# Optimization experiments

Hardware: AMD Instinct MI355X
Metric: run time of the kernel (lower is better)

Reference implementation:

```python
import jax, jax.numpy as jnp
import numpy as np
from jax import lax

D, C, H, W = 4, 64, 64, 64
QK = 32  # q/k projection channels


def _conv3x3(x, w, b):
    # x: [D,C,H,W], w: [O,I,3,3] -> [D,O,H,W], SAME padding, stride 1
    y = lax.conv_general_dilated(x, w, window_strides=(1, 1), padding='SAME',
                                 dimension_numbers=('NCHW', 'OIHW', 'NCHW'))
    return y + b[None, :, None, None]


def setup_inputs() -> dict:
    key = jax.random.key(0)
    ks = jax.random.split(key, 6)
    x = jax.random.normal(ks[0], (D, C, H, W), dtype=jnp.float32)
    atten = jax.random.normal(ks[1], (D, H * W, H * W), dtype=jnp.float32)
    q_w = jax.random.normal(ks[2], (QK, C, 3, 3), dtype=jnp.float32) * 0.05
    q_b = jax.random.normal(ks[3], (QK,), dtype=jnp.float32) * 0.05
    k_w = jax.random.normal(ks[4], (QK, C, 3, 3), dtype=jnp.float32) * 0.05
    k_b = jax.random.normal(ks[5], (QK,), dtype=jnp.float32) * 0.05
    gamma = jnp.ones((1,), dtype=jnp.float32)
    return {"x": x, "atten": atten, "q_w": q_w, "q_b": q_b,
            "k_w": k_w, "k_b": k_b, "gamma": gamma}


def reference(x, atten, q_w, q_b, k_w, k_b, gamma):
    d, c, h, w = x.shape
    n = h * w
    q = _conv3x3(x, q_w, q_b).reshape(d, QK, n)   # [D,32,N]
    k = _conv3x3(x, k_w, k_b).reshape(d, QK, n)   # [D,32,N]
    v = x.reshape(d, c, n)                         # [D,C,N]
    # attention = softmax(q^T k), then softmax(attention + atten) -- double softmax
    attn = jax.nn.softmax(jnp.einsum('dcn,dcm->dnm', q, k), axis=-1)  # [D,N,N]
    attn = jax.nn.softmax(attn + atten, axis=-1)
    # out = v @ attn^T  -> [D,C,N]
    out = jnp.einsum('dcm,dnm->dcn', v, attn).reshape(d, c, h, w)
    return gamma * out + x
```

## Files before the change

### kernel.cpp

```cpp
#include <hip/hip_runtime.h>
#include <hip/hip_bf16.h>

typedef float  f32x4  __attribute__((ext_vector_type(4)));
typedef short  s16x4  __attribute__((ext_vector_type(4)));
typedef short  s16x8  __attribute__((ext_vector_type(8)));
typedef __bf16 bf16x8 __attribute__((ext_vector_type(8)));

#define N_PIX 4096

__device__ __forceinline__ unsigned short f2bf(float f) {
    __hip_bfloat16 h = __float2bfloat16(f);
    return *reinterpret_cast<unsigned short*>(&h);
}
__device__ __forceinline__ float bf2f(unsigned short u) {
    __hip_bfloat16 h;
    *reinterpret_cast<unsigned short*>(&h) = u;
    return __bfloat162float(h);
}

#if __has_builtin(__builtin_amdgcn_mfma_f32_16x16x16bf16_1k)
#define USE_K16 1
#else
#define USE_K16 0
#endif

__device__ __forceinline__ f32x4 mac_k32(s16x4 alo, s16x4 ahi, s16x4 blo, s16x4 bhi, f32x4 c) {
#if USE_K16
    c = __builtin_amdgcn_mfma_f32_16x16x16bf16_1k(alo, blo, c, 0, 0, 0);
    c = __builtin_amdgcn_mfma_f32_16x16x16bf16_1k(ahi, bhi, c, 0, 0, 0);
#else
    s16x8 a8 = __builtin_shufflevector(alo, ahi, 0, 1, 2, 3, 4, 5, 6, 7);
    s16x8 b8 = __builtin_shufflevector(blo, bhi, 0, 1, 2, 3, 4, 5, 6, 7);
    c = __builtin_amdgcn_mfma_f32_16x16x32_bf16(__builtin_bit_cast(bf16x8, a8),
                                                __builtin_bit_cast(bf16x8, b8), c, 0, 0, 0);
#endif
    return c;
}

__global__ __launch_bounds__(256) void to_bf16_kernel(const float* __restrict__ x,
                                                      unsigned short* __restrict__ v_bf) {
    int i = blockIdx.x * 256 + threadIdx.x;
    v_bf[i] = f2bf(x[i]);
}

__global__ __launch_bounds__(256) void pad_kernel(const float* __restrict__ x,
                                                  float* __restrict__ xp) {
    int i = blockIdx.x * 256 + threadIdx.x;
    int xx = i % 66;
    int t  = i / 66;
    int yy = t % 66;
    int cd = t / 66;
    float v = 0.f;
    if (xx >= 1 && xx <= 64 && yy >= 1 && yy <= 64)
        v = x[(size_t)cd * 4096 + (yy - 1) * 64 + (xx - 1)];
    xp[i] = v;
}

__global__ __launch_bounds__(256) void conv_qk_kernel(
    const float* __restrict__ xp,
    const float* __restrict__ q_w, const float* __restrict__ q_b,
    const float* __restrict__ k_w, const float* __restrict__ k_b,
    unsigned short* __restrict__ qTp_hi, unsigned short* __restrict__ qTp_lo,
    unsigned short* __restrict__ kTp_hi, unsigned short* __restrict__ kTp_lo) {
    int bid = blockIdx.x;
    int d  = bid >> 9;
    int o  = __builtin_amdgcn_readfirstlane((bid >> 4) & 31);
    int yg = bid & 15;
    int tid = threadIdx.x;
    int y   = yg * 4 + (tid >> 6);
    int col = tid & 63;
    const float* xc0 = xp + (size_t)d * (64 * 4356) + y * 66 + col;
    const float* wq = q_w + o * 576;
    const float* wk = k_w + o * 576;
    float aq0 = 0.f, aq1 = 0.f, aq2 = 0.f, ak0 = 0.f, ak1 = 0.f, ak2 = 0.f;
#pragma unroll 2
    for (int c = 0; c < 64; ++c) {
        const float* xc = xc0 + c * 4356;
        float x00 = xc[0],   x01 = xc[1],   x02 = xc[2];
        float x10 = xc[66],  x11 = xc[67],  x12 = xc[68];
        float x20 = xc[132], x21 = xc[133], x22 = xc[134];
        const float* wqc = wq + c * 9;
        const float* wkc = wk + c * 9;
        aq0 = fmaf(wqc[0], x00, fmaf(wqc[1], x01, fmaf(wqc[2], x02, aq0)));
        aq1 = fmaf(wqc[3], x10, fmaf(wqc[4], x11, fmaf(wqc[5], x12, aq1)));
        aq2 = fmaf(wqc[6], x20, fmaf(wqc[7], x21, fmaf(wqc[8], x22, aq2)));
        ak0 = fmaf(wkc[0], x00, fmaf(wkc[1], x01, fmaf(wkc[2], x02, ak0)));
        ak1 = fmaf(wkc[3], x10, fmaf(wkc[4], x11, fmaf(wkc[5], x12, ak1)));
        ak2 = fmaf(wkc[6], x20, fmaf(wkc[7], x21, fmaf(wkc[8], x22, ak2)));
    }
    float aq = aq0 + aq1 + aq2 + q_b[o];
    float ak = ak0 + ak1 + ak2 + k_b[o];
    int n = y * 64 + col;
    size_t base = ((size_t)d * N_PIX + n) * 32 + o;
    unsigned short qh = f2bf(aq);
    unsigned short ql = f2bf(aq - bf2f(qh));
    unsigned short kh = f2bf(ak);
    unsigned short kl = f2bf(ak - bf2f(kh));
    qTp_hi[base] = qh; qTp_lo[base] = ql;
    kTp_hi[base] = kh; kTp_lo[base] = kl;
}

__global__ __launch_bounds__(256) void attn_kernel(
    const float* __restrict__ x, const float* __restrict__ atten,
    const float* __restrict__ gamma,
    const unsigned short* __restrict__ qTp_hi, const unsigned short* __restrict__ qTp_lo,
    const unsigned short* __restrict__ kTp_hi, const unsigned short* __restrict__ kTp_lo,
    const unsigned short* __restrict__ v_bf, float* __restrict__ out) {
    __shared__ __align__(16) unsigned short P_s[4][16][68];
    __shared__ float Lred[4][16];
    __shared__ float Ared[4][64][17];

    int tid  = threadIdx.x;
    int lane = tid & 63;
    int w    = tid >> 6;
    int n16 = lane & 15;
    int g   = lane >> 4;
    int bid = blockIdx.x;
    int d   = bid >> 8;
    int rb  = (bid & 255) << 4;
    int nrow = rb + n16;

    size_t qrow = ((size_t)d * N_PIX + nrow) * 32;
    s16x4 qh0 = *(const s16x4*)(qTp_hi + qrow + 4 * g);
    s16x4 qh1 = *(const s16x4*)(qTp_hi + qrow + 16 + 4 * g);
    s16x4 ql0 = *(const s16x4*)(qTp_lo + qrow + 4 * g);
    s16x4 ql1 = *(const s16x4*)(qTp_lo + qrow + 16 + 4 * g);

    const unsigned short* kTh_d = kTp_hi + (size_t)d * N_PIX * 32;
    const unsigned short* kTl_d = kTp_lo + (size_t)d * N_PIX * 32;

    float l1p = 0.f;
    for (int i = 0; i < 16; ++i) {
        int m0 = (i * 4 + w) * 64;
#pragma unroll
        for (int t = 0; t < 4; ++t) {
            size_t krow = (size_t)(m0 + t * 16 + n16) * 32;
            s16x4 kh0 = *(const s16x4*)(kTh_d + krow + 4 * g);
            s16x4 kh1 = *(const s16x4*)(kTh_d + krow + 16 + 4 * g);
            s16x4 kl0 = *(const s16x4*)(kTl_d + krow + 4 * g);
            s16x4 kl1 = *(const s16x4*)(kTl_d + krow + 16 + 4 * g);
            f32x4 s = {0.f, 0.f, 0.f, 0.f};
            s = mac_k32(kh0, kh1, qh0, qh1, s);
            s = mac_k32(kh0, kh1, ql0, ql1, s);
            s = mac_k32(kl0, kl1, qh0, qh1, s);
            l1p += __expf(s[0] - 40.f) + __expf(s[1] - 40.f) +
                   __expf(s[2] - 40.f) + __expf(s[3] - 40.f);
        }
    }
    l1p += __shfl_xor(l1p, 16, 64);
    l1p += __shfl_xor(l1p, 32, 64);
    if (g == 0) Lred[w][n16] = l1p;
    __syncthreads();
    float L1 = Lred[0][n16] + Lred[1][n16] + Lred[2][n16] + Lred[3][n16];
    float rcpL1 = 1.f / L1;

    const float* arow = atten + ((size_t)d << 24) + (size_t)nrow * N_PIX;
    const unsigned short* v_d = v_bf + (size_t)d * 64 * N_PIX;
    float l2p = 0.f;
    f32x4 acco[4];
#pragma unroll
    for (int ct = 0; ct < 4; ++ct) acco[ct] = f32x4{0.f, 0.f, 0.f, 0.f};

    for (int i = 0; i < 16; ++i) {
        int m0 = (i * 4 + w) * 64;
        f32x4 av4[4];
#pragma unroll
        for (int t = 0; t < 4; ++t)
            av4[t] = *(const f32x4*)&arow[m0 + t * 16 + 4 * g];

#pragma unroll
        for (int t = 0; t < 4; ++t) {
            size_t krow = (size_t)(m0 + t * 16 + n16) * 32;
            s16x4 kh0 = *(const s16x4*)(kTh_d + krow + 4 * g);
            s16x4 kh1 = *(const s16x4*)(kTh_d + krow + 16 + 4 * g);
            s16x4 kl0 = *(const s16x4*)(kTl_d + krow + 4 * g);
            s16x4 kl1 = *(const s16x4*)(kTl_d + krow + 16 + 4 * g);
            f32x4 s = {0.f, 0.f, 0.f, 0.f};
            s = mac_k32(kh0, kh1, qh0, qh1, s);
            s = mac_k32(kh0, kh1, ql0, ql1, s);
            s = mac_k32(kl0, kl1, qh0, qh1, s);
#pragma unroll
            for (int r = 0; r < 4; ++r) {
                float attn1 = __expf(s[r] - 40.f) * rcpL1;
                float p = __expf(attn1 + av4[t][r] - 8.f);
                l2p += p;
                P_s[w][n16][t * 16 + 4 * g + r] = f2bf(p);
            }
        }
        asm volatile("" ::: "memory");

#pragma unroll
        for (int h = 0; h < 2; ++h) {
            s16x4 p0 = *(const s16x4*)&P_s[w][n16][h * 32 + 4 * g];
            s16x4 p1 = *(const s16x4*)&P_s[w][n16][h * 32 + 16 + 4 * g];
#pragma unroll
            for (int ct = 0; ct < 4; ++ct) {
                const unsigned short* vr = v_d + (size_t)(ct * 16 + n16) * N_PIX + m0 + h * 32;
                s16x4 v0 = *(const s16x4*)(vr + 4 * g);
                s16x4 v1 = *(const s16x4*)(vr + 16 + 4 * g);
                acco[ct] = mac_k32(v0, v1, p0, p1, acco[ct]);
            }
        }
        asm volatile("" ::: "memory");
    }

    __syncthreads();
    l2p += __shfl_xor(l2p, 16, 64);
    l2p += __shfl_xor(l2p, 32, 64);
    if (g == 0) Lred[w][n16] = l2p;
#pragma unroll
    for (int ct = 0; ct < 4; ++ct)
#pragma unroll
        for (int r = 0; r < 4; ++r)
            Ared[w][lane][ct * 4 + r] = acco[ct][r];
    __syncthreads();

    if (w == 0) {
        float L2 = Lred[0][n16] + Lred[1][n16] + Lred[2][n16] + Lred[3][n16];
        float rcpL2 = 1.f / L2;
        float gam = gamma[0];
#pragma unroll
        for (int ct = 0; ct < 4; ++ct) {
#pragma unroll
            for (int r = 0; r < 4; ++r) {
                int j = ct * 4 + r;
                float tot = Ared[0][lane][j] + Ared[1][lane][j] +
                            Ared[2][lane][j] + Ared[3][lane][j];
                int c = ct * 16 + 4 * g + r;
                size_t idx = ((size_t)(d * 64 + c)) * N_PIX + rb + n16;
                out[idx] = gam * tot * rcpL2 + x[idx];
            }
        }
    }
}

extern "C" void kernel_launch(void* const* d_in, const int* in_sizes, int n_in,
                              void* d_out, int out_size, void* d_ws, size_t ws_size,
                              hipStream_t stream) {
    const float* x     = (const float*)d_in[0];
    const float* atten = (const float*)d_in[1];
    const float* q_w   = (const float*)d_in[2];
    const float* q_b   = (const float*)d_in[3];
    const float* k_w   = (const float*)d_in[4];
    const float* k_b   = (const float*)d_in[5];
    const float* gamma = (const float*)d_in[6];
    float* out = (float*)d_out;

    char* ws = (char*)d_ws;
    const size_t MB = 1u << 20;
    unsigned short* qTp_hi = (unsigned short*)(ws + 0 * MB);
    unsigned short* qTp_lo = (unsigned short*)(ws + 1 * MB);
    unsigned short* kTp_hi = (unsigned short*)(ws + 2 * MB);
    unsigned short* kTp_lo = (unsigned short*)(ws + 3 * MB);
    unsigned short* v_bf   = (unsigned short*)(ws + 4 * MB);
    float*          xp     = (float*)(ws + 8 * MB);

    hipLaunchKernelGGL(to_bf16_kernel, dim3(4096), dim3(256), 0, stream, x, v_bf);
    hipLaunchKernelGGL(pad_kernel, dim3(4356), dim3(256), 0, stream, x, xp);
    hipLaunchKernelGGL(conv_qk_kernel, dim3(2048), dim3(256), 0, stream,
                       xp, q_w, q_b, k_w, k_b, qTp_hi, qTp_lo, kTp_hi, kTp_lo);
    hipLaunchKernelGGL(attn_kernel, dim3(1024), dim3(256), 0, stream,
                       x, atten, gamma, qTp_hi, qTp_lo, kTp_hi, kTp_lo, v_bf, out);
}
```

Measured before the change: 603.3 us.

## Vectorize loads across kernels, double-buffer P tile, interleave batch in block index

Several loosely related changes land together. The bf16 conversion and the conv input reads now use vector loads, and K, Q, V and P are read as 8-wide bf16 vectors, with each wave's K tiles hoisted ahead of the MFMAs. The P staging buffer in LDS is double-buffered and padded so the trailing compiler barrier can go, and the batch index is interleaved into the low block-index bits so concurrently running blocks spread over all four batches. This aims to cut instruction count and memory latency stalls in the attention kernel, at the cost of more registers and LDS.

Result: faster. 530.8 us (-12.0%).

```diff
diff --git a/kernel.cpp b/kernel.cpp
--- a/kernel.cpp
+++ b/kernel.cpp
@@ -2,6 +2,7 @@
 #include <hip/hip_bf16.h>
 
 typedef float  f32x4  __attribute__((ext_vector_type(4)));
+typedef float  f32x4u __attribute__((ext_vector_type(4), aligned(4)));
 typedef short  s16x4  __attribute__((ext_vector_type(4)));
 typedef short  s16x8  __attribute__((ext_vector_type(8)));
 typedef __bf16 bf16x8 __attribute__((ext_vector_type(8)));
@@ -24,13 +25,15 @@
 #define USE_K16 0
 #endif
 
-__device__ __forceinline__ f32x4 mac_k32(s16x4 alo, s16x4 ahi, s16x4 blo, s16x4 bhi, f32x4 c) {
+__device__ __forceinline__ f32x4 mac_k32v(s16x8 a8, s16x8 b8, f32x4 c) {
 #if USE_K16
+    s16x4 alo = __builtin_shufflevector(a8, a8, 0, 1, 2, 3);
+    s16x4 ahi = __builtin_shufflevector(a8, a8, 4, 5, 6, 7);
+    s16x4 blo = __builtin_shufflevector(b8, b8, 0, 1, 2, 3);
+    s16x4 bhi = __builtin_shufflevector(b8, b8, 4, 5, 6, 7);
     c = __builtin_amdgcn_mfma_f32_16x16x16bf16_1k(alo, blo, c, 0, 0, 0);
     c = __builtin_amdgcn_mfma_f32_16x16x16bf16_1k(ahi, bhi, c, 0, 0, 0);
 #else
-    s16x8 a8 = __builtin_shufflevector(alo, ahi, 0, 1, 2, 3, 4, 5, 6, 7);
-    s16x8 b8 = __builtin_shufflevector(blo, bhi, 0, 1, 2, 3, 4, 5, 6, 7);
     c = __builtin_amdgcn_mfma_f32_16x16x32_bf16(__builtin_bit_cast(bf16x8, a8),
                                                 __builtin_bit_cast(bf16x8, b8), c, 0, 0, 0);
 #endif
@@ -40,7 +43,11 @@
 __global__ __launch_bounds__(256) void to_bf16_kernel(const float* __restrict__ x,
                                                       unsigned short* __restrict__ v_bf) {
     int i = blockIdx.x * 256 + threadIdx.x;
-    v_bf[i] = f2bf(x[i]);
+    f32x4 f = *(const f32x4*)(x + i * 4);
+    s16x4 p;
+    p[0] = (short)f2bf(f[0]); p[1] = (short)f2bf(f[1]);
+    p[2] = (short)f2bf(f[2]); p[3] = (short)f2bf(f[3]);
+    *(s16x4*)(v_bf + i * 4) = p;
 }
 
 __global__ __launch_bounds__(256) void pad_kernel(const float* __restrict__ x,
@@ -63,9 +70,10 @@
     unsigned short* __restrict__ qTp_hi, unsigned short* __restrict__ qTp_lo,
     unsigned short* __restrict__ kTp_hi, unsigned short* __restrict__ kTp_lo) {
     int bid = blockIdx.x;
-    int d  = bid >> 9;
-    int o  = __builtin_amdgcn_readfirstlane((bid >> 4) & 31);
-    int yg = bid & 15;
+    int d    = bid & 3;
+    int rest = bid >> 2;
+    int o  = __builtin_amdgcn_readfirstlane(rest & 31);
+    int yg = rest >> 5;
     int tid = threadIdx.x;
     int y   = yg * 4 + (tid >> 6);
     int col = tid & 63;
@@ -73,20 +81,20 @@
     const float* wq = q_w + o * 576;
     const float* wk = k_w + o * 576;
     float aq0 = 0.f, aq1 = 0.f, aq2 = 0.f, ak0 = 0.f, ak1 = 0.f, ak2 = 0.f;
-#pragma unroll 2
+#pragma unroll 4
     for (int c = 0; c < 64; ++c) {
         const float* xc = xc0 + c * 4356;
-        float x00 = xc[0],   x01 = xc[1],   x02 = xc[2];
-        float x10 = xc[66],  x11 = xc[67],  x12 = xc[68];
-        float x20 = xc[132], x21 = xc[133], x22 = xc[134];
+        f32x4u r0 = *(const f32x4u*)(xc);
+        f32x4u r1 = *(const f32x4u*)(xc + 66);
+        f32x4u r2 = *(const f32x4u*)(xc + 132);
         const float* wqc = wq + c * 9;
         const float* wkc = wk + c * 9;
-        aq0 = fmaf(wqc[0], x00, fmaf(wqc[1], x01, fmaf(wqc[2], x02, aq0)));
-        aq1 = fmaf(wqc[3], x10, fmaf(wqc[4], x11, fmaf(wqc[5], x12, aq1)));
-        aq2 = fmaf(wqc[6], x20, fmaf(wqc[7], x21, fmaf(wqc[8], x22, aq2)));
-        ak0 = fmaf(wkc[0], x00, fmaf(wkc[1], x01, fmaf(wkc[2], x02, ak0)));
-        ak1 = fmaf(wkc[3], x10, fmaf(wkc[4], x11, fmaf(wkc[5], x12, ak1)));
-        ak2 = fmaf(wkc[6], x20, fmaf(wkc[7], x21, fmaf(wkc[8], x22, ak2)));
+        aq0 = fmaf(wqc[0], r0[0], fmaf(wqc[1], r0[1], fmaf(wqc[2], r0[2], aq0)));
+        aq1 = fmaf(wqc[3], r1[0], fmaf(wqc[4], r1[1], fmaf(wqc[5], r1[2], aq1)));
+        aq2 = fmaf(wqc[6], r2[0], fmaf(wqc[7], r2[1], fmaf(wqc[8], r2[2], aq2)));
+        ak0 = fmaf(wkc[0], r0[0], fmaf(wkc[1], r0[1], fmaf(wkc[2], r0[2], ak0)));
+        ak1 = fmaf(wkc[3], r1[0], fmaf(wkc[4], r1[1], fmaf(wkc[5], r1[2], ak1)));
+        ak2 = fmaf(wkc[6], r2[0], fmaf(wkc[7], r2[1], fmaf(wkc[8], r2[2], ak2)));
     }
     float aq = aq0 + aq1 + aq2 + q_b[o];
     float ak = ak0 + ak1 + ak2 + k_b[o];
@@ -106,7 +114,7 @@
     const unsigned short* __restrict__ qTp_hi, const unsigned short* __restrict__ qTp_lo,
     const unsigned short* __restrict__ kTp_hi, const unsigned short* __restrict__ kTp_lo,
     const unsigned short* __restrict__ v_bf, float* __restrict__ out) {
-    __shared__ __align__(16) unsigned short P_s[4][16][68];
+    __shared__ __align__(16) unsigned short P_s[4][2][16][72];
     __shared__ float Lred[4][16];
     __shared__ float Ared[4][64][17];
 
@@ -116,15 +124,13 @@
     int n16 = lane & 15;
     int g   = lane >> 4;
     int bid = blockIdx.x;
-    int d   = bid >> 8;
-    int rb  = (bid & 255) << 4;
+    int d   = bid & 3;
+    int rb  = (bid >> 2) << 4;
     int nrow = rb + n16;
 
     size_t qrow = ((size_t)d * N_PIX + nrow) * 32;
-    s16x4 qh0 = *(const s16x4*)(qTp_hi + qrow + 4 * g);
-    s16x4 qh1 = *(const s16x4*)(qTp_hi + qrow + 16 + 4 * g);
-    s16x4 ql0 = *(const s16x4*)(qTp_lo + qrow + 4 * g);
-    s16x4 ql1 = *(const s16x4*)(qTp_lo + qrow + 16 + 4 * g);
+    s16x8 qh8 = *(const s16x8*)(qTp_hi + qrow + 8 * g);
+    s16x8 ql8 = *(const s16x8*)(qTp_lo + qrow + 8 * g);
 
     const unsigned short* kTh_d = kTp_hi + (size_t)d * N_PIX * 32;
     const unsigned short* kTl_d = kTp_lo + (size_t)d * N_PIX * 32;
@@ -132,17 +138,19 @@
     float l1p = 0.f;
     for (int i = 0; i < 16; ++i) {
         int m0 = (i * 4 + w) * 64;
+        s16x8 kh8[4], kl8[4];
 #pragma unroll
         for (int t = 0; t < 4; ++t) {
             size_t krow = (size_t)(m0 + t * 16 + n16) * 32;
-            s16x4 kh0 = *(const s16x4*)(kTh_d + krow + 4 * g);
-            s16x4 kh1 = *(const s16x4*)(kTh_d + krow + 16 + 4 * g);
-            s16x4 kl0 = *(const s16x4*)(kTl_d + krow + 4 * g);
-            s16x4 kl1 = *(const s16x4*)(kTl_d + krow + 16 + 4 * g);
+            kh8[t] = *(const s16x8*)(kTh_d + krow + 8 * g);
+            kl8[t] = *(const s16x8*)(kTl_d + krow + 8 * g);
+        }
+#pragma unroll
+        for (int t = 0; t < 4; ++t) {
             f32x4 s = {0.f, 0.f, 0.f, 0.f};
-            s = mac_k32(kh0, kh1, qh0, qh1, s);
-            s = mac_k32(kh0, kh1, ql0, ql1, s);
-            s = mac_k32(kl0, kl1, qh0, qh1, s);
+            s = mac_k32v(kh8[t], qh8, s);
+            s = mac_k32v(kh8[t], ql8, s);
+            s = mac_k32v(kl8[t], qh8, s);
             l1p += __expf(s[0] - 40.f) + __expf(s[1] - 40.f) +
                    __expf(s[2] - 40.f) + __expf(s[3] - 40.f);
         }
@@ -163,45 +171,46 @@
 
     for (int i = 0; i < 16; ++i) {
         int m0 = (i * 4 + w) * 64;
+        int buf = i & 1;
         f32x4 av4[4];
 #pragma unroll
         for (int t = 0; t < 4; ++t)
             av4[t] = *(const f32x4*)&arow[m0 + t * 16 + 4 * g];
-
+        s16x8 kh8[4], kl8[4];
 #pragma unroll
         for (int t = 0; t < 4; ++t) {
             size_t krow = (size_t)(m0 + t * 16 + n16) * 32;
-            s16x4 kh0 = *(const s16x4*)(kTh_d + krow + 4 * g);
-            s16x4 kh1 = *(const s16x4*)(kTh_d + krow + 16 + 4 * g);
-            s16x4 kl0 = *(const s16x4*)(kTl_d + krow + 4 * g);
-            s16x4 kl1 = *(const s16x4*)(kTl_d + krow + 16 + 4 * g);
+            kh8[t] = *(const s16x8*)(kTh_d + krow + 8 * g);
+            kl8[t] = *(const s16x8*)(kTl_d + krow + 8 * g);
+        }
+#pragma unroll
+        for (int t = 0; t < 4; ++t) {
             f32x4 s = {0.f, 0.f, 0.f, 0.f};
-            s = mac_k32(kh0, kh1, qh0, qh1, s);
-            s = mac_k32(kh0, kh1, ql0, ql1, s);
-            s = mac_k32(kl0, kl1, qh0, qh1, s);
+            s = mac_k32v(kh8[t], qh8, s);
+            s = mac_k32v(kh8[t], ql8, s);
+            s = mac_k32v(kl8[t], qh8, s);
+            s16x4 pp;
 #pragma unroll
             for (int r = 0; r < 4; ++r) {
                 float attn1 = __expf(s[r] - 40.f) * rcpL1;
                 float p = __expf(attn1 + av4[t][r] - 8.f);
                 l2p += p;
-                P_s[w][n16][t * 16 + 4 * g + r] = f2bf(p);
+                pp[r] = (short)f2bf(p);
             }
+            *(s16x4*)&P_s[w][buf][n16][t * 16 + 4 * g] = pp;
         }
         asm volatile("" ::: "memory");
 
 #pragma unroll
         for (int h = 0; h < 2; ++h) {
-            s16x4 p0 = *(const s16x4*)&P_s[w][n16][h * 32 + 4 * g];
-            s16x4 p1 = *(const s16x4*)&P_s[w][n16][h * 32 + 16 + 4 * g];
+            s16x8 p8 = *(const s16x8*)&P_s[w][buf][n16][h * 32 + 8 * g];
 #pragma unroll
             for (int ct = 0; ct < 4; ++ct) {
                 const unsigned short* vr = v_d + (size_t)(ct * 16 + n16) * N_PIX + m0 + h * 32;
-                s16x4 v0 = *(const s16x4*)(vr + 4 * g);
-                s16x4 v1 = *(const s16x4*)(vr + 16 + 4 * g);
-                acco[ct] = mac_k32(v0, v1, p0, p1, acco[ct]);
+                s16x8 v8 = *(const s16x8*)(vr + 8 * g);
+                acco[ct] = mac_k32v(v8, p8, acco[ct]);
             }
         }
-        asm volatile("" ::: "memory");
     }
 
     __syncthreads();
@@ -255,7 +264,7 @@
     unsigned short* v_bf   = (unsigned short*)(ws + 4 * MB);
     float*          xp     = (float*)(ws + 8 * MB);
 
-    hipLaunchKernelGGL(to_bf16_kernel, dim3(4096), dim3(256), 0, stream, x, v_bf);
+    hipLaunchKernelGGL(to_bf16_kernel, dim3(1024), dim3(256), 0, stream, x, v_bf);
     hipLaunchKernelGGL(pad_kernel, dim3(4356), dim3(256), 0, stream, x, xp);
     hipLaunchKernelGGL(conv_qk_kernel, dim3(2048), dim3(256), 0, stream,
                        xp, q_w, q_b, k_w, k_b, qTp_hi, qTp_lo, kTp_hi, kTp_lo);
```
